# Optimization experiments

Hardware: AMD Instinct MI355X
Metric: run time of the kernel (lower is better)

## Reference

```python
import jax, jax.numpy as jnp
import numpy as np

B, T, D, H, F = 2, 2048, 2048, 16, 8192
DH = D // H  # 128
EPS = 1e-6   # flax LayerNorm default


def _layernorm(x, scale, bias):
    mu = jnp.mean(x, axis=-1, keepdims=True)
    var = jnp.mean(jnp.square(x - mu), axis=-1, keepdims=True)
    return (x - mu) * jax.lax.rsqrt(var + EPS) * scale + bias


def setup_inputs() -> dict:
    key = jax.random.key(0)
    ks = jax.random.split(key, 8)
    w = 0.02
    return {
        "x": jax.random.normal(ks[0], (B, T, D), jnp.float32),
        "ln1_scale": jnp.ones((D,), jnp.float32),
        "ln1_bias": jnp.zeros((D,), jnp.float32),
        "w_qkv": jax.random.normal(ks[1], (D, 3 * D), jnp.float32) * w,
        "b_qkv": jnp.zeros((3 * D,), jnp.float32),
        "ln2_scale": jnp.ones((D,), jnp.float32),
        "ln2_bias": jnp.zeros((D,), jnp.float32),
        "w1": jax.random.normal(ks[2], (D, F), jnp.float32) * w,
        "b1": jnp.zeros((F,), jnp.float32),
        "w2": jax.random.normal(ks[3], (F, D), jnp.float32) * w,
        "b2": jnp.zeros((D,), jnp.float32),
    }


def reference(x, ln1_scale, ln1_bias, w_qkv, b_qkv, ln2_scale, ln2_bias, w1, b1, w2, b2):
    # --- pre-LN causal self-attention (training=False -> dropout = identity) ---
    r = _layernorm(x, ln1_scale, ln1_bias)
    qkv = r @ w_qkv + b_qkv                       # [B,T,3D]
    q, k, v = jnp.split(qkv, 3, axis=-1)
    q = q.reshape(B, T, H, DH)
    k = k.reshape(B, T, H, DH)
    v = v.reshape(B, T, H, DH)
    attn = jnp.einsum('bthd,bThd->bhtT', q, k) / jnp.sqrt(jnp.float32(DH))
    causal = jnp.tril(jnp.ones((T, T), bool))
    attn = jnp.where(causal, attn, -jnp.inf)
    attn = jax.nn.softmax(attn, axis=-1)
    out = jnp.einsum('bhtT,bThd->bthd', attn, v).reshape(B, T, D)
    # NOTE: original module has no output projection after attention.
    x = x + out
    # --- MLP block ---
    r = _layernorm(x, ln2_scale, ln2_bias)
    h = jax.nn.gelu(r @ w1 + b1, approximate=True)  # flax nn.gelu default
    x = x + (h @ w2 + b2)
    return x
```

## Files before the change

kernel.cpp:

```cpp
#include <hip/hip_runtime.h>
#include <hip/hip_bf16.h>
#include <stdint.h>
#include <stddef.h>

using bf16_t = __hip_bfloat16;
typedef __attribute__((ext_vector_type(8))) short short8;
typedef __attribute__((ext_vector_type(4))) short short4v;
typedef __attribute__((ext_vector_type(4))) float f32x4;

__device__ __forceinline__ void gload_lds16(const void* g, void* l) {
  __builtin_amdgcn_global_load_lds((const __attribute__((address_space(1))) void*)g,
                                   (__attribute__((address_space(3))) void*)l,
                                   16, 0, 0);
}

__global__ __launch_bounds__(256) void k_transpose_cvt(const float* __restrict__ in,
                                                       bf16_t* __restrict__ out,
                                                       int K, int N) {
  __shared__ float tile[64][65];
  int n0 = blockIdx.x * 64, k0 = blockIdx.y * 64;
  int t = threadIdx.x;
  int tr = t >> 4, tc = t & 15;
#pragma unroll
  for (int i = 0; i < 4; ++i) {
    float4 v = *(const float4*)(in + (size_t)(k0 + tr + i * 16) * N + n0 + tc * 4);
    tile[tr + i * 16][tc * 4 + 0] = v.x;
    tile[tr + i * 16][tc * 4 + 1] = v.y;
    tile[tr + i * 16][tc * 4 + 2] = v.z;
    tile[tr + i * 16][tc * 4 + 3] = v.w;
  }
  __syncthreads();
#pragma unroll
  for (int i = 0; i < 4; ++i) {
    int nn = tr + i * 16;
    short4v s;
    s[0] = (short)__bfloat16_as_ushort(__float2bfloat16(tile[tc * 4 + 0][nn]));
    s[1] = (short)__bfloat16_as_ushort(__float2bfloat16(tile[tc * 4 + 1][nn]));
    s[2] = (short)__bfloat16_as_ushort(__float2bfloat16(tile[tc * 4 + 2][nn]));
    s[3] = (short)__bfloat16_as_ushort(__float2bfloat16(tile[tc * 4 + 3][nn]));
    *(short4v*)(out + (size_t)(n0 + nn) * K + k0 + tc * 4) = s;
  }
}

__global__ __launch_bounds__(256) void k_layernorm(const float* __restrict__ x,
                                                   const float* __restrict__ gam,
                                                   const float* __restrict__ bet,
                                                   bf16_t* __restrict__ out) {
  int row = blockIdx.x, t = threadIdx.x;
  const float4* xr = (const float4*)(x + (size_t)row * 2048);
  float4 a = xr[t], b = xr[t + 256];
  float s  = a.x + a.y + a.z + a.w + b.x + b.y + b.z + b.w;
  float s2 = a.x*a.x + a.y*a.y + a.z*a.z + a.w*a.w
           + b.x*b.x + b.y*b.y + b.z*b.z + b.w*b.w;
#pragma unroll
  for (int off = 32; off >= 1; off >>= 1) {
    s  += __shfl_xor(s, off);
    s2 += __shfl_xor(s2, off);
  }
  __shared__ float red[8];
  if ((t & 63) == 0) { red[t >> 6] = s; red[4 + (t >> 6)] = s2; }
  __syncthreads();
  float S  = red[0] + red[1] + red[2] + red[3];
  float S2 = red[4] + red[5] + red[6] + red[7];
  float mu = S * (1.0f / 2048.0f);
  float var = S2 * (1.0f / 2048.0f) - mu * mu;
  float rstd = rsqrtf(var + 1e-6f);
  const float4* gv = (const float4*)gam;
  const float4* bv = (const float4*)bet;
  float4 g1 = gv[t], g2 = gv[t + 256], c1 = bv[t], c2 = bv[t + 256];
  bf16_t* orow = out + (size_t)row * 2048;
  orow[4*t + 0]    = __float2bfloat16((a.x - mu) * rstd * g1.x + c1.x);
  orow[4*t + 1]    = __float2bfloat16((a.y - mu) * rstd * g1.y + c1.y);
  orow[4*t + 2]    = __float2bfloat16((a.z - mu) * rstd * g1.z + c1.z);
  orow[4*t + 3]    = __float2bfloat16((a.w - mu) * rstd * g1.w + c1.w);
  orow[1024 + 4*t + 0] = __float2bfloat16((b.x - mu) * rstd * g2.x + c2.x);
  orow[1024 + 4*t + 1] = __float2bfloat16((b.y - mu) * rstd * g2.y + c2.y);
  orow[1024 + 4*t + 2] = __float2bfloat16((b.z - mu) * rstd * g2.z + c2.z);
  orow[1024 + 4*t + 3] = __float2bfloat16((b.w - mu) * rstd * g2.w + c2.w);
}

template <int EPI>
__global__ __launch_bounds__(512, 2) void k_gemm8(const bf16_t* __restrict__ A,
                                                  const bf16_t* __restrict__ Bt,
                                                  const float* __restrict__ bias,
                                                  bf16_t* __restrict__ Cb,
                                                  float* __restrict__ Cf,
                                                  bf16_t* __restrict__ Vt,
                                                  int Ndim, int LDA, int LDB,
                                                  int Kdim, int nsub) {
  __shared__ __align__(16) char lds[131072];
  int orig = blockIdx.x;
  int xcd = orig & 7;
  int i = orig >> 3;
  int m = i & 15;
  int j = i >> 4;
  int n_local = j % nsub;
  int chunk = j / nsub;
  int m0 = m * 256;
  int n0 = (xcd * nsub + n_local) * 256;
  int tid = threadIdx.x;
  int w = tid >> 6, lane = tid & 63;
  int lr = lane & 15, lk = lane >> 4;
  int wr = w >> 2, wc = w & 3;

  const bf16_t* Ag = A + (size_t)m0 * LDA + (size_t)chunk * Kdim;
  const bf16_t* Bg = Bt + (size_t)n0 * LDB + (size_t)chunk * Kdim;
  int swch = ((tid & 7) ^ ((tid >> 3) & 7)) << 3;
  const bf16_t* pA0 = Ag + (size_t)(tid >> 3) * LDA + swch;
  const bf16_t* pA1 = pA0 + (size_t)128 * LDA;
  int nb0 = ((tid >> 8) & 1) * 64 + ((tid >> 3) & 31);
  const bf16_t* pB0 = Bg + (size_t)nb0 * LDB + swch;
  const bf16_t* pB1 = pB0 + (size_t)128 * LDB;
  int dstb = tid * 16;
  int chv0 = ((lk)     ^ (lr & 7)) * 16;
  int chv1 = ((4 + lk) ^ (lr & 7)) * 16;
  int aof0 = 65536 + wr * 8192 + lr * 128 + chv0;
  int aof1 = 65536 + wr * 8192 + lr * 128 + chv1;
  int bof0 = wc * 4096 + lr * 128 + chv0;
  int bof1 = wc * 4096 + lr * 128 + chv1;

  f32x4 acc[8][4];
#pragma unroll
  for (int ii = 0; ii < 8; ++ii)
#pragma unroll
    for (int jj = 0; jj < 4; ++jj) acc[ii][jj] = (f32x4){0.f, 0.f, 0.f, 0.f};
  short8 af[4][2], bq0[2][2], bq1[2][2];

#define STAGE_A(p, h, kt) do { \
    size_t ko = (size_t)(kt) * 64 + (size_t)(h) * 64 * LDA; \
    gload_lds16(pA0 + ko, lds + 65536 + (p) * 32768 + (h) * 16384 + dstb); \
    gload_lds16(pA1 + ko, lds + 65536 + (p) * 32768 + (h) * 16384 + 8192 + dstb); } while (0)
#define STAGE_B(p, h, kt) do { \
    size_t ko = (size_t)(kt) * 64 + (size_t)(h) * 32 * LDB; \
    gload_lds16(pB0 + ko, lds + (p) * 32768 + (h) * 16384 + dstb); \
    gload_lds16(pB1 + ko, lds + (p) * 32768 + (h) * 16384 + 8192 + dstb); } while (0)
#define READ_A(p, mh) do { \
    _Pragma("unroll") for (int mf = 0; mf < 4; ++mf) { \
      af[mf][0] = *(const short8*)(lds + (p) * 32768 + (mh) * 16384 + mf * 2048 + aof0); \
      af[mf][1] = *(const short8*)(lds + (p) * 32768 + (mh) * 16384 + mf * 2048 + aof1); } } while (0)
#define READ_B0(p) do { \
    _Pragma("unroll") for (int nf = 0; nf < 2; ++nf) { \
      bq0[nf][0] = *(const short8*)(lds + (p) * 32768 + nf * 2048 + bof0); \
      bq0[nf][1] = *(const short8*)(lds + (p) * 32768 + nf * 2048 + bof1); } } while (0)
#define READ_B1(p) do { \
    _Pragma("unroll") for (int nf = 0; nf < 2; ++nf) { \
      bq1[nf][0] = *(const short8*)(lds + (p) * 32768 + 16384 + nf * 2048 + bof0); \
      bq1[nf][1] = *(const short8*)(lds + (p) * 32768 + 16384 + nf * 2048 + bof1); } } while (0)
#define MM16(mh, nh) do { \
    _Pragma("unroll") for (int ks = 0; ks < 2; ++ks) \
    _Pragma("unroll") for (int mf = 0; mf < 4; ++mf) \
    _Pragma("unroll") for (int nf = 0; nf < 2; ++nf) \
      acc[(mh) * 4 + mf][(nh) * 2 + nf] = __builtin_amdgcn_mfma_f32_16x16x32_bf16( \
          af[mf][ks], (nh) ? bq1[nf][ks] : bq0[nf][ks], \
          acc[(mh) * 4 + mf][(nh) * 2 + nf], 0, 0, 0); } while (0)
#define BARRIER() asm volatile("s_barrier" ::: "memory")
#define LGKM0()  do { asm volatile("s_waitcnt lgkmcnt(0)" ::: "memory"); __builtin_amdgcn_sched_barrier(0); } while (0)
#define PRIO1()  __builtin_amdgcn_s_setprio(1)
#define PRIO0()  __builtin_amdgcn_s_setprio(0)
#define BODY(t, p, S1, S2, VMN) do { \
    READ_A(p, 0); READ_B0(p); \
    if (S1) STAGE_B((p) ^ 1, 0, (t) + 1); \
    asm volatile("s_waitcnt lgkmcnt(8)" ::: "memory"); \
    BARRIER(); LGKM0(); PRIO1(); MM16(0, 0); PRIO0(); BARRIER(); \
    READ_B1(p); \
    if (S2) STAGE_A(p, 0, (t) + 2); \
    BARRIER(); LGKM0(); PRIO1(); MM16(0, 1); PRIO0(); BARRIER(); \
    READ_A(p, 1); \
    if (S2) STAGE_B(p, 1, (t) + 2); \
    BARRIER(); LGKM0(); PRIO1(); MM16(1, 1); PRIO0(); BARRIER(); \
    if (S2) STAGE_A(p, 1, (t) + 2); \
    BARRIER(); PRIO1(); MM16(1, 0); PRIO0(); \
    asm volatile("s_waitcnt vmcnt(%0)" :: "i"(VMN) : "memory"); \
    BARRIER(); } while (0)

  const int NT = Kdim >> 6;
  STAGE_A(0, 0, 0); STAGE_B(0, 0, 0); STAGE_B(0, 1, 0); STAGE_A(0, 1, 0);
  STAGE_A(1, 0, 1); STAGE_B(1, 1, 1); STAGE_A(1, 1, 1);
  asm volatile("s_waitcnt vmcnt(6)" ::: "memory");
  BARRIER();

  int t = 0;
  for (; t + 3 < NT; t += 2) {
    BODY(t, 0, 1, 1, 6);
    BODY(t + 1, 1, 1, 1, 6);
  }
  BODY(t, 0, 1, 0, 0);
  {
    READ_A(1, 0); READ_B0(1);
    BARRIER(); LGKM0(); MM16(0, 0); BARRIER();
    READ_B1(1);
    BARRIER(); LGKM0(); MM16(0, 1); BARRIER();
    READ_A(1, 1);
    BARRIER(); LGKM0(); MM16(1, 1); BARRIER();
    MM16(1, 0);
  }
#undef STAGE_A
#undef STAGE_B
#undef READ_A
#undef READ_B0
#undef READ_B1
#undef MM16
#undef BARRIER
#undef LGKM0
#undef PRIO1
#undef PRIO0
#undef BODY

  if (EPI == 4 && n0 >= 4096) {
#pragma unroll
    for (int mf = 0; mf < 8; ++mf) {
#pragma unroll
      for (int nf = 0; nf < 4; ++nf) {
        int cl = n0 + wc * 64 + nf * 16 + lr;
        int d = cl - 4096;
        int hh = d >> 7, dh = d & 127;
        int rwb = m0 + wr * 128 + mf * 16 + lk * 4;
        int bb = rwb >> 11, tt = rwb & 2047;
        float bs = bias[cl];
        short4v s;
#pragma unroll
        for (int r = 0; r < 4; ++r)
          s[r] = (short)__bfloat16_as_ushort(__float2bfloat16(acc[mf][nf][r] + bs));
        *(short4v*)(Vt + ((size_t)(bb * 16 + hh) * 128 + dh) * 2048 + tt) = s;
      }
    }
    return;
  }
#pragma unroll
  for (int mf = 0; mf < 8; ++mf) {
#pragma unroll
    for (int nf = 0; nf < 4; ++nf) {
#pragma unroll
      for (int r = 0; r < 4; ++r) {
        int rw = m0 + wr * 128 + mf * 16 + lk * 4 + r;
        int cl = n0 + wc * 64 + nf * 16 + lr;
        float v = acc[mf][nf][r];
        size_t gi = (size_t)rw * Ndim + cl;
        if (EPI == 0 || EPI == 4) {
          Cb[gi] = __float2bfloat16(v + bias[cl]);
        } else if (EPI == 1) {
          float vv = v + bias[cl];
          float u = vv * (vv * vv * 0.044715f + 1.0f) * 0.7978845608028654f;
          float gl = 0.5f * vv * (1.0f + tanhf(u));
          Cb[gi] = __float2bfloat16(gl);
        } else {
          float add = v + (chunk == 0 ? bias[cl] : 0.0f);
          atomicAdd(&Cf[gi], add);
        }
      }
    }
  }
}

__global__ __launch_bounds__(256, 2) void k_attn(const bf16_t* __restrict__ qkv,
                                                 const bf16_t* __restrict__ vT,
                                                 const float* __restrict__ x,
                                                 float* __restrict__ out) {
  __shared__ __align__(16) bf16_t Pl[4][32][40];
  int j = blockIdx.x;
  int bh = j & 31;
  int cq = j >> 5;
  int b = bh >> 4, h = bh & 15;
  int w = threadIdx.x >> 6, lane = threadIdx.x & 63;
  int lr = lane & 15, lk = lane >> 4;
  int c = (w == 0) ? cq : (w == 1) ? (63 - cq) : (w == 2) ? (31 - cq) : (32 + cq);
  int q0 = c * 32;
  const bf16_t* qb = qkv + (size_t)(b * 2048) * 6144 + h * 128;
  const bf16_t* kb = qb + 2048;
  const bf16_t* vb = vT + (size_t)(b * 16 + h) * 128 * 2048;
  short8 qf[2][4];
#pragma unroll
  for (int qg = 0; qg < 2; ++qg)
#pragma unroll
    for (int d4 = 0; d4 < 4; ++d4)
      qf[qg][d4] = *(const short8*)(qb + (size_t)(q0 + qg * 16 + lr) * 6144 + d4 * 32 + lk * 8);
  float m[2][4], l[2][4];
#pragma unroll
  for (int qg = 0; qg < 2; ++qg)
#pragma unroll
    for (int r = 0; r < 4; ++r) { m[qg][r] = -1e30f; l[qg][r] = 0.f; }
  f32x4 o[2][8] = {};
  int nkt = c + 1;
  const float sc = 0.08838834764831845f;
  short8 kf[2][4], vf[8];
#pragma unroll
  for (int nt = 0; nt < 2; ++nt)
#pragma unroll
    for (int d4 = 0; d4 < 4; ++d4)
      kf[nt][d4] = *(const short8*)(kb + (size_t)(nt * 16 + lr) * 6144 + d4 * 32 + lk * 8);
#pragma unroll
  for (int d8 = 0; d8 < 8; ++d8)
    vf[d8] = *(const short8*)(vb + (size_t)(d8 * 16 + lr) * 2048 + lk * 8);

  for (int kt = 0; kt < nkt; ++kt) {
    int tk0 = kt * 32;
    f32x4 s[2][2] = {};
    __builtin_amdgcn_s_setprio(1);
#pragma unroll
    for (int d4 = 0; d4 < 4; ++d4)
#pragma unroll
      for (int qg = 0; qg < 2; ++qg)
#pragma unroll
        for (int nt = 0; nt < 2; ++nt)
          s[qg][nt] = __builtin_amdgcn_mfma_f32_16x16x32_bf16(qf[qg][d4], kf[nt][d4], s[qg][nt], 0, 0, 0);
    __builtin_amdgcn_s_setprio(0);
    if (kt + 1 < nkt) {
      int tn = tk0 + 32;
#pragma unroll
      for (int nt = 0; nt < 2; ++nt)
#pragma unroll
        for (int d4 = 0; d4 < 4; ++d4)
          kf[nt][d4] = *(const short8*)(kb + (size_t)(tn + nt * 16 + lr) * 6144 + d4 * 32 + lk * 8);
    }
#pragma unroll
    for (int qg = 0; qg < 2; ++qg) {
      float sv[2][4], mt[4];
#pragma unroll
      for (int r = 0; r < 4; ++r) {
        int qr = q0 + qg * 16 + lk * 4 + r;
#pragma unroll
        for (int nt = 0; nt < 2; ++nt) {
          float v = s[qg][nt][r] * sc;
          int kc = tk0 + nt * 16 + lr;
          sv[nt][r] = (kc > qr) ? -1e30f : v;
        }
        mt[r] = fmaxf(sv[0][r], sv[1][r]);
      }
#pragma unroll
      for (int off = 1; off < 16; off <<= 1)
#pragma unroll
        for (int r = 0; r < 4; ++r) mt[r] = fmaxf(mt[r], __shfl_xor(mt[r], off));
      float alpha[4], rs[4];
#pragma unroll
      for (int r = 0; r < 4; ++r) {
        float mn = fmaxf(m[qg][r], mt[r]);
        alpha[r] = __expf(m[qg][r] - mn);
        m[qg][r] = mn;
      }
#pragma unroll
      for (int r = 0; r < 4; ++r) {
        float p0 = __expf(sv[0][r] - m[qg][r]);
        float p1 = __expf(sv[1][r] - m[qg][r]);
        rs[r] = p0 + p1;
        Pl[w][qg * 16 + lk * 4 + r][lr]      = __float2bfloat16(p0);
        Pl[w][qg * 16 + lk * 4 + r][16 + lr] = __float2bfloat16(p1);
      }
#pragma unroll
      for (int off = 1; off < 16; off <<= 1)
#pragma unroll
        for (int r = 0; r < 4; ++r) rs[r] += __shfl_xor(rs[r], off);
#pragma unroll
      for (int r = 0; r < 4; ++r) l[qg][r] = l[qg][r] * alpha[r] + rs[r];
#pragma unroll
      for (int d8 = 0; d8 < 8; ++d8)
#pragma unroll
        for (int r = 0; r < 4; ++r) o[qg][d8][r] *= alpha[r];
    }
    asm volatile("s_waitcnt lgkmcnt(0)" ::: "memory");
    short8 pf[2];
#pragma unroll
    for (int qg = 0; qg < 2; ++qg)
      pf[qg] = *(const short8*)(&Pl[w][qg * 16 + lr][lk * 8]);
    __builtin_amdgcn_s_setprio(1);
#pragma unroll
    for (int d8 = 0; d8 < 8; ++d8)
#pragma unroll
      for (int qg = 0; qg < 2; ++qg)
        o[qg][d8] = __builtin_amdgcn_mfma_f32_16x16x32_bf16(pf[qg], vf[d8], o[qg][d8], 0, 0, 0);
    __builtin_amdgcn_s_setprio(0);
    if (kt + 1 < nkt) {
      int tn = tk0 + 32;
#pragma unroll
      for (int d8 = 0; d8 < 8; ++d8)
        vf[d8] = *(const short8*)(vb + (size_t)(d8 * 16 + lr) * 2048 + tn + lk * 8);
    }
  }
#pragma unroll
  for (int qg = 0; qg < 2; ++qg)
#pragma unroll
    for (int d8 = 0; d8 < 8; ++d8)
#pragma unroll
      for (int r = 0; r < 4; ++r) {
        int qr = q0 + qg * 16 + lk * 4 + r;
        int cl = h * 128 + d8 * 16 + lr;
        size_t gi = (size_t)(b * 2048 + qr) * 2048 + cl;
        out[gi] = x[gi] + o[qg][d8][r] / l[qg][r];
      }
}

extern "C" void kernel_launch(void* const* d_in, const int* in_sizes, int n_in,
                              void* d_out, int out_size, void* d_ws, size_t ws_size,
                              hipStream_t stream) {
  const float* x    = (const float*)d_in[0];
  const float* ln1s = (const float*)d_in[1];
  const float* ln1b = (const float*)d_in[2];
  const float* wqkv = (const float*)d_in[3];
  const float* bqkv = (const float*)d_in[4];
  const float* ln2s = (const float*)d_in[5];
  const float* ln2b = (const float*)d_in[6];
  const float* w1   = (const float*)d_in[7];
  const float* b1   = (const float*)d_in[8];
  const float* w2   = (const float*)d_in[9];
  const float* b2   = (const float*)d_in[10];
  float* out = (float*)d_out;
  char* ws = (char*)d_ws;

  bf16_t* r     = (bf16_t*)(ws + 0);
  bf16_t* qkv   = (bf16_t*)(ws + 16777216);
  bf16_t* w1T   = (bf16_t*)(ws + 67108864);
  bf16_t* w2T   = (bf16_t*)(ws + 100663296);
  bf16_t* h     = (bf16_t*)(ws + 134217728);
  bf16_t* wqkvT = (bf16_t*)(ws + 134217728);
  bf16_t* vT    = (bf16_t*)(ws + 167772160);

  k_transpose_cvt<<<dim3(96, 32),  256, 0, stream>>>(wqkv, wqkvT, 2048, 6144);
  k_transpose_cvt<<<dim3(128, 32), 256, 0, stream>>>(w1,   w1T,   2048, 8192);
  k_transpose_cvt<<<dim3(32, 128), 256, 0, stream>>>(w2,   w2T,   8192, 2048);
  k_layernorm<<<4096, 256, 0, stream>>>(x, ln1s, ln1b, r);
  k_gemm8<4><<<384, 512, 0, stream>>>(r, wqkvT, bqkv, qkv, nullptr, vT, 6144, 2048, 2048, 2048, 3);
  k_attn<<<512, 256, 0, stream>>>(qkv, vT, x, out);
  k_layernorm<<<4096, 256, 0, stream>>>(out, ln2s, ln2b, r);
  k_gemm8<1><<<512, 512, 0, stream>>>(r, w1T, b1, h, nullptr, nullptr, 8192, 2048, 2048, 2048, 4);
  k_gemm8<3><<<256, 512, 0, stream>>>(h, w2T, b2, nullptr, out, nullptr, 2048, 8192, 8192, 4096, 1);
}
```

Measured before the change: 648.5 us.

## Replace 256x256 GEMM with 128x128 tile kernel loading B directly to registers

Replaces the 512-thread 256x256-tile GEMM with a 256-thread 128x128-tile kernel. The A tile is staged into LDS through a triple-buffered ring, while B fragments are loaded straight from global memory into registers and double-buffered across k-tiles. The aim is to cut LDS traffic and barrier overhead and to launch four times as many blocks for better occupancy and load balance. In exchange, each block gets less data reuse from its smaller tile, and the per-lane B loads may be less coalesced.

```diff
diff --git a/kernel.cpp b/kernel.cpp
--- a/kernel.cpp
+++ b/kernel.cpp
@@ -80,141 +80,124 @@
 }
 
 template <int EPI>
-__global__ __launch_bounds__(512, 2) void k_gemm8(const bf16_t* __restrict__ A,
-                                                  const bf16_t* __restrict__ Bt,
-                                                  const float* __restrict__ bias,
-                                                  bf16_t* __restrict__ Cb,
-                                                  float* __restrict__ Cf,
-                                                  bf16_t* __restrict__ Vt,
-                                                  int Ndim, int LDA, int LDB,
-                                                  int Kdim, int nsub) {
-  __shared__ __align__(16) char lds[131072];
+__global__ __launch_bounds__(256, 2) void k_gemm10(const bf16_t* __restrict__ A,
+                                                   const bf16_t* __restrict__ Bt,
+                                                   const float* __restrict__ bias,
+                                                   bf16_t* __restrict__ Cb,
+                                                   float* __restrict__ Cf,
+                                                   bf16_t* __restrict__ Vt,
+                                                   int Ndim, int LDA, int LDB,
+                                                   int Kdim, int nsub) {
+  __shared__ __align__(16) char lds[49152];
   int orig = blockIdx.x;
   int xcd = orig & 7;
   int i = orig >> 3;
-  int m = i & 15;
-  int j = i >> 4;
+  int m = i & 31;
+  int j = i >> 5;
   int n_local = j % nsub;
   int chunk = j / nsub;
-  int m0 = m * 256;
-  int n0 = (xcd * nsub + n_local) * 256;
+  int m0 = m * 128;
+  int n0 = (xcd * nsub + n_local) * 128;
   int tid = threadIdx.x;
   int w = tid >> 6, lane = tid & 63;
   int lr = lane & 15, lk = lane >> 4;
-  int wr = w >> 2, wc = w & 3;
+  int wr = w >> 1, wc = w & 1;
 
   const bf16_t* Ag = A + (size_t)m0 * LDA + (size_t)chunk * Kdim;
   const bf16_t* Bg = Bt + (size_t)n0 * LDB + (size_t)chunk * Kdim;
-  int swch = ((tid & 7) ^ ((tid >> 3) & 7)) << 3;
-  const bf16_t* pA0 = Ag + (size_t)(tid >> 3) * LDA + swch;
-  const bf16_t* pA1 = pA0 + (size_t)128 * LDA;
-  int nb0 = ((tid >> 8) & 1) * 64 + ((tid >> 3) & 31);
-  const bf16_t* pB0 = Bg + (size_t)nb0 * LDB + swch;
-  const bf16_t* pB1 = pB0 + (size_t)128 * LDB;
+  int swz = ((tid & 7) ^ ((tid >> 3) & 7)) << 3;
+  const bf16_t* pA0 = Ag + (size_t)((tid >> 3) +  0) * LDA + swz;
+  const bf16_t* pA1 = Ag + (size_t)((tid >> 3) + 32) * LDA + swz;
+  const bf16_t* pA2 = Ag + (size_t)((tid >> 3) + 64) * LDA + swz;
+  const bf16_t* pA3 = Ag + (size_t)((tid >> 3) + 96) * LDA + swz;
   int dstb = tid * 16;
-  int chv0 = ((lk)     ^ (lr & 7)) * 16;
-  int chv1 = ((4 + lk) ^ (lr & 7)) * 16;
-  int aof0 = 65536 + wr * 8192 + lr * 128 + chv0;
-  int aof1 = 65536 + wr * 8192 + lr * 128 + chv1;
-  int bof0 = wc * 4096 + lr * 128 + chv0;
-  int bof1 = wc * 4096 + lr * 128 + chv1;
-
-  f32x4 acc[8][4];
-#pragma unroll
-  for (int ii = 0; ii < 8; ++ii)
+  const bf16_t* pB0 = Bg + (size_t)(wc * 64 +  0 + lr) * LDB + lk * 8;
+  const bf16_t* pB1 = Bg + (size_t)(wc * 64 + 16 + lr) * LDB + lk * 8;
+  const bf16_t* pB2 = Bg + (size_t)(wc * 64 + 32 + lr) * LDB + lk * 8;
+  const bf16_t* pB3 = Bg + (size_t)(wc * 64 + 48 + lr) * LDB + lk * 8;
+  int ch0 = ((lk)     ^ (lr & 7)) * 16;
+  int ch1 = ((4 + lk) ^ (lr & 7)) * 16;
+  int arow[4];
+#pragma unroll
+  for (int mf = 0; mf < 4; ++mf) arow[mf] = (wr * 64 + mf * 16 + lr) * 128;
+
+  f32x4 acc[4][4];
+#pragma unroll
+  for (int ii = 0; ii < 4; ++ii)
 #pragma unroll
     for (int jj = 0; jj < 4; ++jj) acc[ii][jj] = (f32x4){0.f, 0.f, 0.f, 0.f};
-  short8 af[4][2], bq0[2][2], bq1[2][2];
-
-#define STAGE_A(p, h, kt) do { \
-    size_t ko = (size_t)(kt) * 64 + (size_t)(h) * 64 * LDA; \
-    gload_lds16(pA0 + ko, lds + 65536 + (p) * 32768 + (h) * 16384 + dstb); \
-    gload_lds16(pA1 + ko, lds + 65536 + (p) * 32768 + (h) * 16384 + 8192 + dstb); } while (0)
-#define STAGE_B(p, h, kt) do { \
-    size_t ko = (size_t)(kt) * 64 + (size_t)(h) * 32 * LDB; \
-    gload_lds16(pB0 + ko, lds + (p) * 32768 + (h) * 16384 + dstb); \
-    gload_lds16(pB1 + ko, lds + (p) * 32768 + (h) * 16384 + 8192 + dstb); } while (0)
-#define READ_A(p, mh) do { \
-    _Pragma("unroll") for (int mf = 0; mf < 4; ++mf) { \
-      af[mf][0] = *(const short8*)(lds + (p) * 32768 + (mh) * 16384 + mf * 2048 + aof0); \
-      af[mf][1] = *(const short8*)(lds + (p) * 32768 + (mh) * 16384 + mf * 2048 + aof1); } } while (0)
-#define READ_B0(p) do { \
-    _Pragma("unroll") for (int nf = 0; nf < 2; ++nf) { \
-      bq0[nf][0] = *(const short8*)(lds + (p) * 32768 + nf * 2048 + bof0); \
-      bq0[nf][1] = *(const short8*)(lds + (p) * 32768 + nf * 2048 + bof1); } } while (0)
-#define READ_B1(p) do { \
-    _Pragma("unroll") for (int nf = 0; nf < 2; ++nf) { \
-      bq1[nf][0] = *(const short8*)(lds + (p) * 32768 + 16384 + nf * 2048 + bof0); \
-      bq1[nf][1] = *(const short8*)(lds + (p) * 32768 + 16384 + nf * 2048 + bof1); } } while (0)
-#define MM16(mh, nh) do { \
-    _Pragma("unroll") for (int ks = 0; ks < 2; ++ks) \
-    _Pragma("unroll") for (int mf = 0; mf < 4; ++mf) \
-    _Pragma("unroll") for (int nf = 0; nf < 2; ++nf) \
-      acc[(mh) * 4 + mf][(nh) * 2 + nf] = __builtin_amdgcn_mfma_f32_16x16x32_bf16( \
-          af[mf][ks], (nh) ? bq1[nf][ks] : bq0[nf][ks], \
-          acc[(mh) * 4 + mf][(nh) * 2 + nf], 0, 0, 0); } while (0)
-#define BARRIER() asm volatile("s_barrier" ::: "memory")
-#define LGKM0()  do { asm volatile("s_waitcnt lgkmcnt(0)" ::: "memory"); __builtin_amdgcn_sched_barrier(0); } while (0)
-#define PRIO1()  __builtin_amdgcn_s_setprio(1)
-#define PRIO0()  __builtin_amdgcn_s_setprio(0)
-#define BODY(t, p, S1, S2, VMN) do { \
-    READ_A(p, 0); READ_B0(p); \
-    if (S1) STAGE_B((p) ^ 1, 0, (t) + 1); \
-    asm volatile("s_waitcnt lgkmcnt(8)" ::: "memory"); \
-    BARRIER(); LGKM0(); PRIO1(); MM16(0, 0); PRIO0(); BARRIER(); \
-    READ_B1(p); \
-    if (S2) STAGE_A(p, 0, (t) + 2); \
-    BARRIER(); LGKM0(); PRIO1(); MM16(0, 1); PRIO0(); BARRIER(); \
-    READ_A(p, 1); \
-    if (S2) STAGE_B(p, 1, (t) + 2); \
-    BARRIER(); LGKM0(); PRIO1(); MM16(1, 1); PRIO0(); BARRIER(); \
-    if (S2) STAGE_A(p, 1, (t) + 2); \
-    BARRIER(); PRIO1(); MM16(1, 0); PRIO0(); \
+  short8 bqA[4][2], bqB[4][2];
+
+#define STAGEA(off) do { \
+    gload_lds16(pA0, lds + (off) + dstb);          \
+    gload_lds16(pA1, lds + (off) + 4096 + dstb);   \
+    gload_lds16(pA2, lds + (off) + 8192 + dstb);   \
+    gload_lds16(pA3, lds + (off) + 12288 + dstb);  \
+    pA0 += 64; pA1 += 64; pA2 += 64; pA3 += 64; } while (0)
+#define LOADB(SET) do { \
+    SET[0][0] = *(const short8*)(pB0);      SET[0][1] = *(const short8*)(pB0 + 32); \
+    SET[1][0] = *(const short8*)(pB1);      SET[1][1] = *(const short8*)(pB1 + 32); \
+    SET[2][0] = *(const short8*)(pB2);      SET[2][1] = *(const short8*)(pB2 + 32); \
+    SET[3][0] = *(const short8*)(pB3);      SET[3][1] = *(const short8*)(pB3 + 32); \
+    pB0 += 64; pB1 += 64; pB2 += 64; pB3 += 64; } while (0)
+#define KS(SET, ks, CH) do { \
+    short8 af0 = *(const short8*)(lds + rd + arow[0] + (CH)); \
+    short8 af1 = *(const short8*)(lds + rd + arow[1] + (CH)); \
+    short8 af2 = *(const short8*)(lds + rd + arow[2] + (CH)); \
+    short8 af3 = *(const short8*)(lds + rd + arow[3] + (CH)); \
+    _Pragma("unroll") for (int nf = 0; nf < 4; ++nf) { \
+      acc[0][nf] = __builtin_amdgcn_mfma_f32_16x16x32_bf16(af0, SET[nf][ks], acc[0][nf], 0, 0, 0); \
+      acc[1][nf] = __builtin_amdgcn_mfma_f32_16x16x32_bf16(af1, SET[nf][ks], acc[1][nf], 0, 0, 0); \
+      acc[2][nf] = __builtin_amdgcn_mfma_f32_16x16x32_bf16(af2, SET[nf][ks], acc[2][nf], 0, 0, 0); \
+      acc[3][nf] = __builtin_amdgcn_mfma_f32_16x16x32_bf16(af3, SET[nf][ks], acc[3][nf], 0, 0, 0); } } while (0)
+#define ENDTILE(VMN) do { \
+    asm volatile("s_waitcnt lgkmcnt(0)" ::: "memory"); \
     asm volatile("s_waitcnt vmcnt(%0)" :: "i"(VMN) : "memory"); \
-    BARRIER(); } while (0)
-
+    asm volatile("s_barrier" ::: "memory"); \
+    rd = (rd == 32768) ? 0 : rd + 16384; \
+    wrb = (wrb == 32768) ? 0 : wrb + 16384; } while (0)
+
+  int rd = 0, wrb = 32768;
   const int NT = Kdim >> 6;
-  STAGE_A(0, 0, 0); STAGE_B(0, 0, 0); STAGE_B(0, 1, 0); STAGE_A(0, 1, 0);
-  STAGE_A(1, 0, 1); STAGE_B(1, 1, 1); STAGE_A(1, 1, 1);
-  asm volatile("s_waitcnt vmcnt(6)" ::: "memory");
-  BARRIER();
-
-  int t = 0;
-  for (; t + 3 < NT; t += 2) {
-    BODY(t, 0, 1, 1, 6);
-    BODY(t + 1, 1, 1, 1, 6);
-  }
-  BODY(t, 0, 1, 0, 0);
+  STAGEA(0);
+  LOADB(bqA);
+  STAGEA(16384);
+  asm volatile("s_waitcnt vmcnt(12)" ::: "memory");
+  asm volatile("s_barrier" ::: "memory");
+
+  for (int t = 0; t < NT - 2; t += 2) {
+    LOADB(bqB);
+    STAGEA(wrb);
+    KS(bqA, 0, ch0); KS(bqA, 1, ch1);
+    ENDTILE(12);
+    LOADB(bqA);
+    STAGEA(wrb);
+    KS(bqB, 0, ch0); KS(bqB, 1, ch1);
+    ENDTILE(12);
+  }
   {
-    READ_A(1, 0); READ_B0(1);
-    BARRIER(); LGKM0(); MM16(0, 0); BARRIER();
-    READ_B1(1);
-    BARRIER(); LGKM0(); MM16(0, 1); BARRIER();
-    READ_A(1, 1);
-    BARRIER(); LGKM0(); MM16(1, 1); BARRIER();
-    MM16(1, 0);
-  }
-#undef STAGE_A
-#undef STAGE_B
-#undef READ_A
-#undef READ_B0
-#undef READ_B1
-#undef MM16
-#undef BARRIER
-#undef LGKM0
-#undef PRIO1
-#undef PRIO0
-#undef BODY
+    LOADB(bqB);
+    KS(bqA, 0, ch0); KS(bqA, 1, ch1);
+    ENDTILE(8);
+  }
+  {
+    KS(bqB, 0, ch0); KS(bqB, 1, ch1);
+    asm volatile("s_waitcnt lgkmcnt(0)" ::: "memory");
+  }
+#undef STAGEA
+#undef LOADB
+#undef KS
+#undef ENDTILE
 
   if (EPI == 4 && n0 >= 4096) {
 #pragma unroll
-    for (int mf = 0; mf < 8; ++mf) {
+    for (int mf = 0; mf < 4; ++mf) {
 #pragma unroll
       for (int nf = 0; nf < 4; ++nf) {
         int cl = n0 + wc * 64 + nf * 16 + lr;
         int d = cl - 4096;
         int hh = d >> 7, dh = d & 127;
-        int rwb = m0 + wr * 128 + mf * 16 + lk * 4;
+        int rwb = m0 + wr * 64 + mf * 16 + lk * 4;
         int bb = rwb >> 11, tt = rwb & 2047;
         float bs = bias[cl];
         short4v s;
@@ -227,12 +210,12 @@
     return;
   }
 #pragma unroll
-  for (int mf = 0; mf < 8; ++mf) {
+  for (int mf = 0; mf < 4; ++mf) {
 #pragma unroll
     for (int nf = 0; nf < 4; ++nf) {
 #pragma unroll
       for (int r = 0; r < 4; ++r) {
-        int rw = m0 + wr * 128 + mf * 16 + lk * 4 + r;
+        int rw = m0 + wr * 64 + mf * 16 + lk * 4 + r;
         int cl = n0 + wc * 64 + nf * 16 + lr;
         float v = acc[mf][nf][r];
         size_t gi = (size_t)rw * Ndim + cl;
@@ -417,9 +400,9 @@
   k_transpose_cvt<<<dim3(128, 32), 256, 0, stream>>>(w1,   w1T,   2048, 8192);
   k_transpose_cvt<<<dim3(32, 128), 256, 0, stream>>>(w2,   w2T,   8192, 2048);
   k_layernorm<<<4096, 256, 0, stream>>>(x, ln1s, ln1b, r);
-  k_gemm8<4><<<384, 512, 0, stream>>>(r, wqkvT, bqkv, qkv, nullptr, vT, 6144, 2048, 2048, 2048, 3);
+  k_gemm10<4><<<1536, 256, 0, stream>>>(r, wqkvT, bqkv, qkv, nullptr, vT, 6144, 2048, 2048, 2048, 6);
   k_attn<<<512, 256, 0, stream>>>(qkv, vT, x, out);
   k_layernorm<<<4096, 256, 0, stream>>>(out, ln2s, ln2b, r);
-  k_gemm8<1><<<512, 512, 0, stream>>>(r, w1T, b1, h, nullptr, nullptr, 8192, 2048, 2048, 2048, 4);
-  k_gemm8<3><<<256, 512, 0, stream>>>(h, w2T, b2, nullptr, out, nullptr, 2048, 8192, 8192, 4096, 1);
-}
+  k_gemm10<1><<<2048, 256, 0, stream>>>(r, w1T, b1, h, nullptr, nullptr, 8192, 2048, 2048, 2048, 8);
+  k_gemm10<3><<<1024, 256, 0, stream>>>(h, w2T, b2, nullptr, out, nullptr, 2048, 8192, 8192, 4096, 2);
+}
```

New measurement: 1.023 ms. 57.7% more time.
